# Kernel optimization log

Measured on AMD Instinct MI355X. Metric: run time of the kernel, lower is better.

## Reference

```python
import jax, jax.numpy as jnp
import numpy as np

B, S, P, D, H = 2, 1024, 1024, 2048, 16
DH = D // H
QMAX = 127.0


def quantize(x):
    # per-tensor abs-max int8 quantization, matching torch quantize(bits=8)
    scale = jnp.max(jnp.abs(x)) / QMAX
    x_q = jnp.clip(jnp.round(x / scale), -128.0, 127.0).astype(jnp.int8)
    return x_q, scale


def dequantize(x_q, scale):
    return x_q.astype(jnp.float32) * scale


def setup_inputs() -> dict:
    key = jax.random.key(0)
    ks = jax.random.split(key, 12)
    sd = 1.0 / np.sqrt(D)
    inp = {
        'hidden_states': jax.random.normal(ks[0], (B, S, D), jnp.float32),
        'Wq': jax.random.normal(ks[1], (D, D), jnp.float32) * sd,
        'bq': jnp.zeros((D,), jnp.float32),
        'Wk': jax.random.normal(ks[2], (D, D), jnp.float32) * sd,
        'bk': jnp.zeros((D,), jnp.float32),
        'Wv': jax.random.normal(ks[3], (D, D), jnp.float32) * sd,
        'bv': jnp.zeros((D,), jnp.float32),
        'Wo': jax.random.normal(ks[4], (D, D), jnp.float32) * sd,
        'bo': jnp.zeros((D,), jnp.float32),
        'past_k_q': jax.random.randint(ks[5], (B, P, D), -128, 128).astype(jnp.int8),
        'past_k_scale': jnp.float32(0.03),
        'past_v_q': jax.random.randint(ks[6], (B, P, D), -128, 128).astype(jnp.int8),
        'past_v_scale': jnp.float32(0.02),
    }
    return inp


def attention(h, k, v, Wq, bq, Wo, bo):
    # standard causal MHA; query positions are offset by the cache length P
    T = k.shape[1]  # P + S
    q = (h @ Wq + bq).reshape(B, S, H, DH)
    kh = k.reshape(B, T, H, DH)
    vh = v.reshape(B, T, H, DH)
    scores = jnp.einsum('bshd,bthd->bhst', q, kh) / np.sqrt(DH)  # [B,H,S,T]
    causal = jnp.arange(T)[None, :] <= (P + jnp.arange(S))[:, None]  # [S,T]
    scores = jnp.where(causal[None, None], scores, jnp.float32(-1e30))
    attn = jax.nn.softmax(scores, axis=-1)
    out = jnp.einsum('bhst,bthd->bshd', attn, vh).reshape(B, S, D)
    return out @ Wo + bo


def reference(hidden_states, Wq, bq, Wk, bk, Wv, bv, Wo, bo,
              past_k_q, past_k_scale, past_v_q, past_v_scale):
    k = hidden_states @ Wk + bk  # [B,S,D]
    v = hidden_states @ Wv + bv
    k_q, k_scale = quantize(k)
    v_q, v_scale = quantize(v)
    # dequantize cached KV and concat along the sequence dim (dim=1)
    k_prev = dequantize(past_k_q, past_k_scale)
    v_prev = dequantize(past_v_q, past_v_scale)
    k_full = jnp.concatenate([k_prev, k], axis=1)  # [B,P+S,D]
    v_full = jnp.concatenate([v_prev, v], axis=1)
    out = attention(hidden_states, k_full, v_full, Wq, bq, Wo, bo)
    return out, k_q, k_scale, v_q, v_scale
```

## Files before the change

kernel.cpp:

```cpp
#include <hip/hip_runtime.h>

#define SOFT_SCALE 0.08838834764831845f
#define BSD 4194304
#define NELEM 4194304

typedef __attribute__((ext_vector_type(4))) float    f32x4;
typedef __attribute__((ext_vector_type(8))) short    bf16x8;
typedef __attribute__((ext_vector_type(4))) short    bf16x4;
typedef __attribute__((ext_vector_type(4))) unsigned u32x4;

__device__ __forceinline__ float bs2f(short s) {
    unsigned u = ((unsigned)(unsigned short)s) << 16;
    return __builtin_bit_cast(float, u);
}
__device__ __forceinline__ short f2bs(float f) {
    unsigned u = __builtin_bit_cast(unsigned, f);
    unsigned r = (u + 0x7fffu + ((u >> 16) & 1u)) >> 16;
    return (short)r;
}

__device__ __forceinline__ void stage16(const short* g, short* l) {
#if __has_builtin(__builtin_amdgcn_global_load_lds)
    __builtin_amdgcn_global_load_lds(
        (const __attribute__((address_space(1))) void*)g,
        (__attribute__((address_space(3))) void*)l, 16, 0, 0);
#else
    *(bf16x8*)l = *(const bf16x8*)g;
#endif
}

__global__ void probe_init(const int* __restrict__ q, float* __restrict__ scal) {
    const int lane = threadIdx.x;
    int bad = 0;
#pragma unroll
    for (int i = 0; i < 4; ++i) {
        const int v = q[i * 64 + lane];
        bad |= (v < -128 || v > 127) ? 1 : 0;
    }
    const int anybad = __any(bad);
    if (lane == 0) ((int*)scal)[2] = anybad ? 0 : 1;
    if (lane == 1) scal[0] = 0.f;
    if (lane == 2) scal[1] = 0.f;
}

__global__ void prep_kernel(const float* __restrict__ X, short* __restrict__ Y,
                            const void* __restrict__ pk, const void* __restrict__ pv,
                            const float* __restrict__ psk, const float* __restrict__ psv,
                            short* __restrict__ Kf, short* __restrict__ Vf,
                            const int* __restrict__ wsflag) {
    const int z = blockIdx.z;
    const int stride = gridDim.x * blockDim.x;
    if (z == 0) {
        for (int i = blockIdx.x * blockDim.x + threadIdx.x; i < NELEM / 8; i += stride) {
            const int e = i * 8;
            f32x4 a = *(const f32x4*)&X[e];
            f32x4 b = *(const f32x4*)&X[e + 4];
            bf16x8 o;
            o[0] = f2bs(a[0]); o[1] = f2bs(a[1]); o[2] = f2bs(a[2]); o[3] = f2bs(a[3]);
            o[4] = f2bs(b[0]); o[5] = f2bs(b[1]); o[6] = f2bs(b[2]); o[7] = f2bs(b[3]);
            *(bf16x8*)&Y[e] = o;
        }
    } else {
        const void* src = (z == 2) ? pv : pk;
        const float sc = (z == 2) ? *psv : *psk;
        short* dst = (z == 2) ? Vf : Kf;
        const int flag = wsflag[2];
        for (int i = blockIdx.x * blockDim.x + threadIdx.x; i < NELEM / 8; i += stride) {
            const int e = i * 8;
            int vals[8];
            if (flag) {
                const int* s = (const int*)src + e;
                *(int4*)&vals[0] = *(const int4*)&s[0];
                *(int4*)&vals[4] = *(const int4*)&s[4];
            } else {
                const int2 wv = *(const int2*)((const char*)src + e);
#pragma unroll
                for (int j = 0; j < 4; ++j) vals[j] = (int)(signed char)(wv.x >> (8 * j));
#pragma unroll
                for (int j = 0; j < 4; ++j) vals[4 + j] = (int)(signed char)(wv.y >> (8 * j));
            }
            bf16x8 o;
#pragma unroll
            for (int j = 0; j < 8; ++j) o[j] = f2bs((float)vals[j] * sc);
            *(bf16x8*)&dst[e + ((e >> 21) << 21)] = o;
        }
    }
}

__global__ __launch_bounds__(256) void transpose_conv(const float* __restrict__ W0,
                                                      const float* __restrict__ W1,
                                                      const float* __restrict__ W2,
                                                      const float* __restrict__ W3,
                                                      short* __restrict__ WT) {
    __shared__ __align__(16) short Tl[64 * 68];
    const float* W = blockIdx.z == 0 ? W0 : (blockIdx.z == 1 ? W1 :
                     (blockIdx.z == 2 ? W2 : W3));
    short* out = WT + (long)blockIdx.z * 4194304;
    const int tid = threadIdx.x;
    const int n0 = blockIdx.x * 64, k0 = blockIdx.y * 64;
#pragma unroll
    for (int i = 0; i < 4; ++i) {
        const int e = i * 1024 + tid * 4;
        const int r = e >> 6, c = e & 63;
        f32x4 f = *(const f32x4*)&W[(long)(k0 + r) * 2048 + n0 + c];
        bf16x4 s4 = { f2bs(f[0]), f2bs(f[1]), f2bs(f[2]), f2bs(f[3]) };
        *(bf16x4*)&Tl[r * 68 + c] = s4;
    }
    __syncthreads();
#pragma unroll
    for (int i = 0; i < 4; ++i) {
        const int e = i * 1024 + tid * 4;
        const int nr = e >> 6, kk = e & 63;
        bf16x4 o = { Tl[(kk + 0) * 68 + nr], Tl[(kk + 1) * 68 + nr],
                     Tl[(kk + 2) * 68 + nr], Tl[(kk + 3) * 68 + nr] };
        *(bf16x4*)&out[(long)(n0 + nr) * 2048 + k0 + kk] = o;
    }
}

__global__ __launch_bounds__(512, 2) void gemm_qkv8(
    const short* __restrict__ A,
    const short* __restrict__ Bt0, const short* __restrict__ Bt1, const short* __restrict__ Bt2,
    const float* __restrict__ bi0, const float* __restrict__ bi1, const float* __restrict__ bi2,
    void* __restrict__ o0, void* __restrict__ o1, void* __restrict__ o2) {
    __shared__ __align__(16) short L[2][16384];

    const int orig = blockIdx.x + 8 * (blockIdx.y + 8 * blockIdx.z);
    int swz = (orig & 7) * 24 + (orig >> 3);
    const int bx = swz & 7; swz >>= 3;
    const int by = swz & 7;
    const int bz = swz >> 3;

    const short* Bt   = bz == 0 ? Bt0 : (bz == 1 ? Bt1 : Bt2);
    const float* bias = bz == 0 ? bi0 : (bz == 1 ? bi1 : bi2);
    void* outp        = bz == 0 ? o0  : (bz == 1 ? o1  : o2);
    const int mode    = (bz == 0) ? 1 : 2;
    const float scl   = (bz == 0) ? SOFT_SCALE : 1.f;

    const int tid = threadIdx.x, lane = tid & 63, w = tid >> 6;
    const int wm = w >> 2, wn = w & 3;
    const int l4 = lane >> 4, ln = lane & 15;
    const int m0 = by * 256, n0 = bx * 256;

    const int srow = tid >> 2;
    const int scol = (tid & 3) * 8;
    const short* gA0 = A  + (long)(m0 + srow) * 2048 + scol;
    const short* gA1 = A  + (long)(m0 + srow + 128) * 2048 + scol;
    const short* gB0 = Bt + (long)(n0 + srow) * 2048 + scol;
    const short* gB1 = Bt + (long)(n0 + srow + 128) * 2048 + scol;
    const int w0 = srow * 32 + (scol ^ ((srow & 3) << 3));

    const int aswz = (l4 * 8) ^ ((ln & 3) << 3);

    f32x4 acc[8][4];
#pragma unroll
    for (int mi = 0; mi < 8; ++mi)
#pragma unroll
        for (int ni = 0; ni < 4; ++ni) acc[mi][ni] = (f32x4){0, 0, 0, 0};

    bf16x8 g0, g1, g2, g3;
#define LOADG(t)                                   \
    do {                                           \
        const int ko = (t) * 32;                   \
        g0 = *(const bf16x8*)(gA0 + ko);           \
        g1 = *(const bf16x8*)(gA1 + ko);           \
        g2 = *(const bf16x8*)(gB0 + ko);           \
        g3 = *(const bf16x8*)(gB1 + ko);           \
    } while (0)
#define WRITEL(c)                                  \
    do {                                           \
        *(bf16x8*)&L[c][w0] = g0;                  \
        *(bf16x8*)&L[c][w0 + 4096] = g1;           \
        *(bf16x8*)&L[c][8192 + w0] = g2;           \
        *(bf16x8*)&L[c][8192 + w0 + 4096] = g3;    \
    } while (0)

    LOADG(0); WRITEL(0);
    LOADG(1); WRITEL(1);
    LOADG(2);
    __syncthreads();

    for (int s = 0; s < 64; ++s) {
        const int c = s & 1;
        bf16x8 af[8], bfq[4];
#pragma unroll
        for (int fm = 0; fm < 8; ++fm)
            af[fm] = *(const bf16x8*)&L[c][(wm * 128 + fm * 16 + ln) * 32 + aswz];
#pragma unroll
        for (int fn = 0; fn < 4; ++fn)
            bfq[fn] = *(const bf16x8*)&L[c][8192 + (wn * 64 + fn * 16 + ln) * 32 + aswz];
        __builtin_amdgcn_s_setprio(1);
#pragma unroll
        for (int fm = 0; fm < 8; ++fm)
#pragma unroll
            for (int fn = 0; fn < 4; ++fn)
                acc[fm][fn] = __builtin_amdgcn_mfma_f32_16x16x32_bf16(
                    af[fm], bfq[fn], acc[fm][fn], 0, 0, 0);
        __builtin_amdgcn_s_setprio(0);
        asm volatile("s_waitcnt lgkmcnt(0)" ::: "memory");
        __builtin_amdgcn_s_barrier();
        if (s < 62) WRITEL(c);
        if (s < 61) LOADG(s + 3);
        asm volatile("s_waitcnt lgkmcnt(0)" ::: "memory");
    }
#undef LOADG
#undef WRITEL

#pragma unroll
    for (int fn = 0; fn < 4; ++fn) {
        const int gn = n0 + wn * 64 + fn * 16 + ln;
        const float bv = bias[gn];
#pragma unroll
        for (int fm = 0; fm < 8; ++fm) {
#pragma unroll
            for (int r = 0; r < 4; ++r) {
                const int gm = m0 + wm * 128 + fm * 16 + l4 * 4 + r;
                const float v = (acc[fm][fn][r] + bv) * scl;
                if (mode == 1) {
                    ((short*)outp)[(long)gm * 2048 + gn] = f2bs(v);
                } else {
                    const int gr = gm + 1024 + ((gm >> 10) << 10);
                    ((short*)outp)[(long)gr * 2048 + gn] = f2bs(v);
                }
            }
        }
    }
}

__global__ __launch_bounds__(256, 2) void gemm_m97(
    const short* __restrict__ A, const short* __restrict__ Bt,
    const float* __restrict__ bias, void* __restrict__ outp,
    int mode, float scl) {
    __shared__ __align__(16) short Al[2][4096];
    __shared__ __align__(16) short Bl[2][4096];
    const int nbx = gridDim.x, nby = gridDim.y;
    const int nwg = nbx * nby;
    const int orig = blockIdx.x + nbx * blockIdx.y;
    const int cpx = nwg >> 3;
    int swz = (orig & 7) * cpx + (orig >> 3);
    const int bx = swz % nbx;
    const int by = swz / nbx;

    const int tid = threadIdx.x, lane = tid & 63, w = tid >> 6;
    const int wm = w >> 1, wn = w & 1, l4 = lane >> 4, ln = lane & 15;
    const int m0 = by * 128, n0 = bx * 128;

    const short* gA0 = A  + (long)(m0 + (tid >> 2)) * 2048 + (tid & 3) * 8;
    const short* gA1 = gA0 + 64 * 2048;
    const short* gB0 = Bt + (long)(n0 + (tid >> 2)) * 2048 + (tid & 3) * 8;
    const short* gB1 = gB0 + 64 * 2048;

    f32x4 acc[4][4];
#pragma unroll
    for (int mi = 0; mi < 4; ++mi)
#pragma unroll
        for (int ni = 0; ni < 4; ++ni) acc[mi][ni] = (f32x4){0, 0, 0, 0};

#define STAGE_G(buf, ko)                                   \
    do {                                                   \
        stage16(gA0 + (ko), &Al[buf][tid * 8]);            \
        stage16(gA1 + (ko), &Al[buf][2048 + tid * 8]);     \
        stage16(gB0 + (ko), &Bl[buf][tid * 8]);            \
        stage16(gB1 + (ko), &Bl[buf][2048 + tid * 8]);     \
    } while (0)

    STAGE_G(0, 0);
    asm volatile("s_waitcnt vmcnt(0)" ::: "memory");
    __syncthreads();
    int cur = 0;
    for (int kt = 0; kt < 64; ++kt) {
        if (kt < 63) STAGE_G(cur ^ 1, (kt + 1) * 32);
        bf16x8 af[4], bfr[4];
#pragma unroll
        for (int mi = 0; mi < 4; ++mi)
            af[mi] = *(const bf16x8*)&Al[cur][(wm * 64 + mi * 16 + ln) * 32 + l4 * 8];
#pragma unroll
        for (int ni = 0; ni < 4; ++ni)
            bfr[ni] = *(const bf16x8*)&Bl[cur][(wn * 64 + ni * 16 + ln) * 32 + l4 * 8];
#pragma unroll
        for (int mi = 0; mi < 4; ++mi)
#pragma unroll
            for (int ni = 0; ni < 4; ++ni)
                acc[mi][ni] = __builtin_amdgcn_mfma_f32_16x16x32_bf16(
                    af[mi], bfr[ni], acc[mi][ni], 0, 0, 0);
        asm volatile("s_waitcnt vmcnt(0)" ::: "memory");
        __syncthreads();
        cur ^= 1;
    }
#undef STAGE_G

#pragma unroll
    for (int ni = 0; ni < 4; ++ni) {
        const int gn = n0 + wn * 64 + ni * 16 + ln;
        const float bv = bias[gn];
#pragma unroll
        for (int mi = 0; mi < 4; ++mi) {
#pragma unroll
            for (int r = 0; r < 4; ++r) {
                const int gm = m0 + wm * 64 + mi * 16 + l4 * 4 + r;
                const float v = (acc[mi][ni][r] + bv) * scl;
                if (mode == 0) {
                    ((float*)outp)[(long)gm * 2048 + gn] = v;
                } else if (mode == 1) {
                    ((short*)outp)[(long)gm * 2048 + gn] = f2bs(v);
                } else {
                    const int gr = gm + 1024 + ((gm >> 10) << 10);
                    ((short*)outp)[(long)gr * 2048 + gn] = f2bs(v);
                }
            }
        }
    }
}

__global__ __launch_bounds__(256, 2) void gemm_wo(const short* __restrict__ A,
                                                  const short* __restrict__ Bt,
                                                  const float* __restrict__ bias,
                                                  float* __restrict__ outp) {
    __shared__ __align__(16) short Al[2][4096];
    __shared__ __align__(16) short Bl[2][2048];
    const int orig = blockIdx.x + 32 * blockIdx.y;
    const int swz = (orig & 7) * 64 + (orig >> 3);
    const int bx = swz & 31, by = swz >> 5;
    const int tid = threadIdx.x, lane = tid & 63, w = tid >> 6;
    const int wm = w >> 1, wn = w & 1, l4 = lane >> 4, ln = lane & 15;
    const int m0 = by * 128, n0 = bx * 64;

    const short* gA0 = A  + (long)(m0 + (tid >> 2)) * 2048 + (tid & 3) * 8;
    const short* gA1 = gA0 + 64 * 2048;
    const short* gB0 = Bt + (long)(n0 + (tid >> 2)) * 2048 + (tid & 3) * 8;

    f32x4 acc[4][2];
#pragma unroll
    for (int mi = 0; mi < 4; ++mi)
#pragma unroll
        for (int ni = 0; ni < 2; ++ni) acc[mi][ni] = (f32x4){0, 0, 0, 0};

#define STAGE_W(buf, ko)                                   \
    do {                                                   \
        stage16(gA0 + (ko), &Al[buf][tid * 8]);            \
        stage16(gA1 + (ko), &Al[buf][2048 + tid * 8]);     \
        stage16(gB0 + (ko), &Bl[buf][tid * 8]);            \
    } while (0)

    STAGE_W(0, 0);
    asm volatile("s_waitcnt vmcnt(0)" ::: "memory");
    __syncthreads();
    int cur = 0;
    for (int kt = 0; kt < 64; ++kt) {
        if (kt < 63) STAGE_W(cur ^ 1, (kt + 1) * 32);
        bf16x8 af[4], bfr[2];
#pragma unroll
        for (int mi = 0; mi < 4; ++mi)
            af[mi] = *(const bf16x8*)&Al[cur][(wm * 64 + mi * 16 + ln) * 32 + l4 * 8];
#pragma unroll
        for (int ni = 0; ni < 2; ++ni)
            bfr[ni] = *(const bf16x8*)&Bl[cur][(wn * 32 + ni * 16 + ln) * 32 + l4 * 8];
#pragma unroll
        for (int mi = 0; mi < 4; ++mi)
#pragma unroll
            for (int ni = 0; ni < 2; ++ni)
                acc[mi][ni] = __builtin_amdgcn_mfma_f32_16x16x32_bf16(
                    af[mi], bfr[ni], acc[mi][ni], 0, 0, 0);
        asm volatile("s_waitcnt vmcnt(0)" ::: "memory");
        __syncthreads();
        cur ^= 1;
    }
#undef STAGE_W

#pragma unroll
    for (int ni = 0; ni < 2; ++ni) {
        const int gn = n0 + wn * 32 + ni * 16 + ln;
        const float bv = bias[gn];
#pragma unroll
        for (int mi = 0; mi < 4; ++mi) {
#pragma unroll
            for (int r = 0; r < 4; ++r) {
                const int gm = m0 + wm * 64 + mi * 16 + l4 * 4 + r;
                outp[(long)gm * 2048 + gn] = acc[mi][ni][r] + bv;
            }
        }
    }
}

__global__ void absmax_kernel(const short* __restrict__ Kf, const short* __restrict__ Vf,
                              float* __restrict__ scal) {
    const int z = blockIdx.z;
    const short* src = z ? Vf : Kf;
    const int tid = threadIdx.x, lane = tid & 63, w = tid >> 6;
    float mx = 0.f;
    const int stride = gridDim.x * blockDim.x;
    for (int i = blockIdx.x * blockDim.x + tid; i < NELEM / 8; i += stride) {
        const int e = i * 8;
        const int flat = e + 2097152 + ((e >> 21) << 21);
        bf16x8 v = *(const bf16x8*)&src[flat];
#pragma unroll
        for (int j = 0; j < 8; ++j) mx = fmaxf(mx, fabsf(bs2f(v[j])));
    }
#pragma unroll
    for (int o = 32; o > 0; o >>= 1) mx = fmaxf(mx, __shfl_xor(mx, o));
    __shared__ float wred[4];
    if (lane == 0) wred[w] = mx;
    __syncthreads();
    if (tid == 0) {
        const float m2 = fmaxf(fmaxf(wred[0], wred[1]), fmaxf(wred[2], wred[3]));
        atomicMax((unsigned int*)&scal[z], __builtin_bit_cast(unsigned int, m2));
    }
}

__global__ void quantize_kernel(const short* __restrict__ Kf, const short* __restrict__ Vf,
                                const float* __restrict__ scal, float* __restrict__ out) {
    const int z = blockIdx.z;
    const short* src = z ? Vf : Kf;
    const float mx = scal[z];
    const float scale = mx * (1.f / 127.f);
    const float inv = (mx > 0.f) ? 127.f / mx : 0.f;
    const long ob = z ? (2L * BSD + 1) : (1L * BSD);
    if (blockIdx.x == 0 && threadIdx.x == 0)
        out[z ? (3L * BSD + 1) : (2L * BSD)] = scale;
    const int stride = gridDim.x * blockDim.x;
    for (int i = blockIdx.x * blockDim.x + threadIdx.x; i < NELEM / 4; i += stride) {
        const int e = i * 4;
        const int flat = e + 2097152 + ((e >> 21) << 21);
        bf16x4 x4 = *(const bf16x4*)&src[flat];
        float4 q;
        q.x = fminf(127.f, fmaxf(-128.f, rintf(bs2f(x4[0]) * inv)));
        q.y = fminf(127.f, fmaxf(-128.f, rintf(bs2f(x4[1]) * inv)));
        q.z = fminf(127.f, fmaxf(-128.f, rintf(bs2f(x4[2]) * inv)));
        q.w = fminf(127.f, fmaxf(-128.f, rintf(bs2f(x4[3]) * inv)));
        *(float4*)&out[ob + e] = q;
    }
}

__global__ __launch_bounds__(256, 2) void attn_kernel(const short* __restrict__ Q,
                                                      const short* __restrict__ Kf,
                                                      const short* __restrict__ Vf,
                                                      short* __restrict__ O) {
    __shared__ __align__(16) short Kl[2][64 * 136];
    __shared__ __align__(16) short Vt[2][128 * 72];
    const int L = blockIdx.x + 16 * (blockIdx.y + 16 * blockIdx.z);
    const int x = L & 7, rr = L >> 3;
    const int qt0 = rr & 15, pgrp = rr >> 4;
    const int p = x + 8 * pgrp;
    const int h = p >> 1, b = p & 1;
    const int qt = (pgrp >= 2) ? (15 - qt0) : qt0;

    const int tid = threadIdx.x, w = tid >> 6, lane = tid & 63;
    const int l4 = lane >> 4, n = lane & 15;
    const int rg = tid >> 4, cg = tid & 15, stc = cg * 8;
    const int sIdx = qt * 64 + w * 16 + n;
    const int qlim = 1024 + sIdx;

    bf16x8 qf[4];
#pragma unroll
    for (int c = 0; c < 4; ++c)
        qf[c] = *(const bf16x8*)&Q[(long)(b * 1024 + sIdx) * 2048 + h * 128 + c * 32 + l4 * 8];

    f32x4 acco[8];
#pragma unroll
    for (int i = 0; i < 8; ++i) acco[i] = (f32x4){0, 0, 0, 0};
    float m_run = 0.f, l_run = 0.f;

    const short* Kb = Kf + (long)(b * 2048) * 2048 + h * 128;
    const short* Vb = Vf + (long)(b * 2048) * 2048 + h * 128;
    const int nt = 17 + qt;

    bf16x8 kreg[4], vreg[4];
#define LOAD_KV(te)                                                                   \
    do {                                                                              \
        _Pragma("unroll")                                                             \
        for (int i = 0; i < 4; ++i)                                                   \
            kreg[i] = *(const bf16x8*)&Kb[(long)((te) + i * 16 + rg) * 2048 + stc];   \
        _Pragma("unroll")                                                             \
        for (int i = 0; i < 4; ++i)                                                   \
            vreg[i] = *(const bf16x8*)&Vb[(long)((te) + rg * 4 + i) * 2048 + stc];    \
    } while (0)
#define WRITE_BUF(bf)                                                                 \
    do {                                                                              \
        _Pragma("unroll")                                                             \
        for (int i = 0; i < 4; ++i)                                                   \
            *(bf16x8*)&Kl[bf][(i * 16 + rg) * 136 + stc] = kreg[i];                   \
        _Pragma("unroll")                                                             \
        for (int j = 0; j < 8; ++j) {                                                 \
            const int d = stc + j;                                                    \
            bf16x4 c4 = { vreg[0][j], vreg[1][j], vreg[2][j], vreg[3][j] };           \
            *(bf16x4*)&Vt[bf][d * 72 + ((rg ^ ((d >> 3) & 7)) << 2)] = c4;            \
        }                                                                             \
    } while (0)

    LOAD_KV(0);
    WRITE_BUF(0);
    __syncthreads();

    for (int t = 0; t < nt; ++t) {
        const int buf = t & 1;
        const int t0 = t * 64;
        if (t + 1 < nt) LOAD_KV((t + 1) * 64);

        float p16[16];
        __builtin_amdgcn_s_setprio(1);
#pragma unroll
        for (int kt = 0; kt < 4; ++kt) {
            f32x4 sc4 = (f32x4){0, 0, 0, 0};
#pragma unroll
            for (int c = 0; c < 4; ++c) {
                bf16x8 kfr = *(const bf16x8*)&Kl[buf][(kt * 16 + n) * 136 + c * 32 + l4 * 8];
                sc4 = __builtin_amdgcn_mfma_f32_16x16x32_bf16(kfr, qf[c], sc4, 0, 0, 0);
            }
#pragma unroll
            for (int r = 0; r < 4; ++r) p16[kt * 4 + r] = sc4[r];
        }
        __builtin_amdgcn_s_setprio(0);
        if (t >= 16) {
#pragma unroll
            for (int i = 0; i < 16; ++i) {
                const int kg = t0 + (i >> 2) * 16 + l4 * 4 + (i & 3);
                if (kg > qlim) p16[i] = -1e30f;
            }
        }

        float tmax = fmaxf(p16[0], p16[1]);
#pragma unroll
        for (int i = 2; i < 16; ++i) tmax = fmaxf(tmax, p16[i]);
        tmax = fmaxf(tmax, __shfl_xor(tmax, 16));
        tmax = fmaxf(tmax, __shfl_xor(tmax, 32));
        float e16[16], tsum = 0.f;
#pragma unroll
        for (int i = 0; i < 16; ++i) { e16[i] = __expf(p16[i] - m_run); tsum += e16[i]; }
        if (!__all(tmax <= m_run + 8.f)) {
            const float mnew = fmaxf(m_run, tmax);
            const float fac = __expf(m_run - mnew);
            tsum *= fac;
#pragma unroll
            for (int i = 0; i < 16; ++i) e16[i] *= fac;
            l_run *= fac;
#pragma unroll
            for (int i = 0; i < 8; ++i) acco[i] *= fac;
            m_run = mnew;
        }
        tsum += __shfl_xor(tsum, 16);
        tsum += __shfl_xor(tsum, 32);
        l_run += tsum;

        u32x4 pw0, pw1;
#pragma unroll
        for (int wd = 0; wd < 4; ++wd) {
            unsigned r0, r1;
            asm("v_cvt_pk_bf16_f32 %0, %1, %2" : "=v"(r0) : "v"(e16[2 * wd]), "v"(e16[2 * wd + 1]));
            asm("v_cvt_pk_bf16_f32 %0, %1, %2" : "=v"(r1) : "v"(e16[8 + 2 * wd]), "v"(e16[8 + 2 * wd + 1]));
            pw0[wd] = r0; pw1[wd] = r1;
        }
        bf16x8 pb[2] = { __builtin_bit_cast(bf16x8, pw0), __builtin_bit_cast(bf16x8, pw1) };

        __builtin_amdgcn_s_setprio(1);
#pragma unroll
        for (int dc = 0; dc < 8; ++dc) {
            const int d = dc * 16 + n;
            const int swd = ((d >> 3) & 7) << 2;
#pragma unroll
            for (int k32 = 0; k32 < 2; ++k32) {
                bf16x4 g0 = *(const bf16x4*)&Vt[buf][d * 72 + (k32 * 32 + ((4 * l4) ^ swd))];
                bf16x4 g1 = *(const bf16x4*)&Vt[buf][d * 72 + (k32 * 32 + ((16 + 4 * l4) ^ swd))];
                bf16x8 vf = { g0[0], g0[1], g0[2], g0[3], g1[0], g1[1], g1[2], g1[3] };
                acco[dc] = __builtin_amdgcn_mfma_f32_16x16x32_bf16(vf, pb[k32], acco[dc], 0, 0, 0);
            }
        }
        __builtin_amdgcn_s_setprio(0);

        if (t + 1 < nt) WRITE_BUF(buf ^ 1);
        __syncthreads();
    }
#undef LOAD_KV
#undef WRITE_BUF

    const float inv = 1.f / l_run;
#pragma unroll
    for (int dc = 0; dc < 8; ++dc)
#pragma unroll
        for (int r = 0; r < 4; ++r)
            Kl[0][(w * 16 + n) * 136 + dc * 16 + l4 * 4 + r] = f2bs(acco[dc][r] * inv);
    __syncthreads();
#pragma unroll
    for (int i = 0; i < 4; ++i) {
        const int row = i * 4 + (lane >> 4);
        const int col = (lane & 15) * 8;
        bf16x8 ov = *(const bf16x8*)&Kl[0][(w * 16 + row) * 136 + col];
        *(bf16x8*)&O[(long)(b * 1024 + qt * 64 + w * 16 + row) * 2048 + h * 128 + col] = ov;
    }
}

extern "C" void kernel_launch(void* const* d_in, const int* in_sizes, int n_in,
                              void* d_out, int out_size, void* d_ws, size_t ws_size,
                              hipStream_t stream) {
    const float* h   = (const float*)d_in[0];
    const float* Wq  = (const float*)d_in[1];
    const float* bq  = (const float*)d_in[2];
    const float* Wk  = (const float*)d_in[3];
    const float* bk  = (const float*)d_in[4];
    const float* Wv  = (const float*)d_in[5];
    const float* bv  = (const float*)d_in[6];
    const float* Wo  = (const float*)d_in[7];
    const float* bo  = (const float*)d_in[8];
    const void*  pkq = d_in[9];
    const float* pks = (const float*)d_in[10];
    const void*  pvq = d_in[11];
    const float* pvs = (const float*)d_in[12];
    float* out = (float*)d_out;

    char* ws = (char*)d_ws;
    dim3 blk(256);

    if (ws_size >= 83886336ull) {
        float* scal  = (float*)ws;
        short* hbf   = (short*)(ws + 256);
        short* WT4   = (short*)(ws + 256 + 1L * 8388608);
        short* Qbf   = (short*)(ws + 256 + 5L * 8388608);
        short* Kfull = (short*)(ws + 256 + 6L * 8388608);
        short* Vfull = (short*)(ws + 256 + 6L * 8388608 + 16777216);
        short* attnb = hbf;

        probe_init<<<1, 64, 0, stream>>>((const int*)pkq, scal);
        prep_kernel<<<dim3(256, 1, 3), blk, 0, stream>>>(h, hbf, pkq, pvq, pks, pvs,
                                                         Kfull, Vfull, (const int*)d_ws);
        transpose_conv<<<dim3(32, 32, 4), blk, 0, stream>>>(Wq, Wk, Wv, Wo, WT4);
        gemm_qkv8<<<dim3(8, 8, 3), dim3(512), 0, stream>>>(hbf, WT4, WT4 + 4194304,
                                                           WT4 + 8388608, bq, bk, bv,
                                                           Qbf, Kfull, Vfull);
        absmax_kernel<<<dim3(512, 1, 2), blk, 0, stream>>>(Kfull, Vfull, scal);
        quantize_kernel<<<dim3(256, 1, 2), blk, 0, stream>>>(Kfull, Vfull, scal, out);
        attn_kernel<<<dim3(16, 16, 2), blk, 0, stream>>>(Qbf, Kfull, Vfull, attnb);
        gemm_wo<<<dim3(32, 16), blk, 0, stream>>>(attnb, WT4 + 12582912, bo, out);
    } else {
        float* scal  = (float*)ws;
        short* hbf   = (short*)(ws + 256);
        short* WT    = (short*)(ws + 256 + 1L * 8388608);
        short* Qbf   = (short*)(ws + 256 + 2L * 8388608);
        short* Kfull = (short*)(ws + 256 + 3L * 8388608);
        short* Vfull = (short*)(ws + 256 + 3L * 8388608 + 16777216);
        short* attnb = hbf;

        probe_init<<<1, 64, 0, stream>>>((const int*)pkq, scal);
        prep_kernel<<<dim3(256, 1, 3), blk, 0, stream>>>(h, hbf, pkq, pvq, pks, pvs,
                                                         Kfull, Vfull, (const int*)d_ws);
        transpose_conv<<<dim3(32, 32, 1), blk, 0, stream>>>(Wk, Wk, Wk, Wk, WT);
        gemm_m97<<<dim3(16, 16), blk, 0, stream>>>(hbf, WT, bk, Kfull, 2, 1.f);
        transpose_conv<<<dim3(32, 32, 1), blk, 0, stream>>>(Wv, Wv, Wv, Wv, WT);
        gemm_m97<<<dim3(16, 16), blk, 0, stream>>>(hbf, WT, bv, Vfull, 2, 1.f);
        absmax_kernel<<<dim3(512, 1, 2), blk, 0, stream>>>(Kfull, Vfull, scal);
        quantize_kernel<<<dim3(256, 1, 2), blk, 0, stream>>>(Kfull, Vfull, scal, out);
        transpose_conv<<<dim3(32, 32, 1), blk, 0, stream>>>(Wq, Wq, Wq, Wq, WT);
        gemm_m97<<<dim3(16, 16), blk, 0, stream>>>(hbf, WT, bq, Qbf, 1, SOFT_SCALE);
        attn_kernel<<<dim3(16, 16, 2), blk, 0, stream>>>(Qbf, Kfull, Vfull, attnb);
        transpose_conv<<<dim3(32, 32, 1), blk, 0, stream>>>(Wo, Wo, Wo, Wo, WT);
        gemm_wo<<<dim3(32, 16), blk, 0, stream>>>(attnb, WT, bo, out);
    }
}
```

Baseline: 219.0 us.

## Switch QKV GEMM to direct global-to-LDS loads with 4-stage pipeline

```diff
diff --git a/kernel.cpp b/kernel.cpp
--- a/kernel.cpp
+++ b/kernel.cpp
@@ -122,7 +122,7 @@
     const short* __restrict__ Bt0, const short* __restrict__ Bt1, const short* __restrict__ Bt2,
     const float* __restrict__ bi0, const float* __restrict__ bi1, const float* __restrict__ bi2,
     void* __restrict__ o0, void* __restrict__ o1, void* __restrict__ o2) {
-    __shared__ __align__(16) short L[2][16384];
+    __shared__ __align__(16) short L[4][16384];
 
     const int orig = blockIdx.x + 8 * (blockIdx.y + 8 * blockIdx.z);
     int swz = (orig & 7) * 24 + (orig >> 3);
@@ -141,15 +141,22 @@
     const int l4 = lane >> 4, ln = lane & 15;
     const int m0 = by * 256, n0 = bx * 256;
 
-    const int srow = tid >> 2;
     const int scol = (tid & 3) * 8;
-    const short* gA0 = A  + (long)(m0 + srow) * 2048 + scol;
-    const short* gA1 = A  + (long)(m0 + srow + 128) * 2048 + scol;
-    const short* gB0 = Bt + (long)(n0 + srow) * 2048 + scol;
-    const short* gB1 = Bt + (long)(n0 + srow + 128) * 2048 + scol;
-    const int w0 = srow * 32 + (scol ^ ((srow & 3) << 3));
-
-    const int aswz = (l4 * 8) ^ ((ln & 3) << 3);
+    const short* gA = A  + (long)(m0 + (tid >> 2)) * 2048 + scol;
+    const short* gB = Bt + (long)(n0 + (tid >> 2)) * 2048 + scol;
+
+#define ISSUE_A(t)                                                        \
+    do {                                                                  \
+        const long ko = (long)(t) * 32;                                   \
+        stage16(gA + ko,              &L[(t) & 3][tid * 8]);              \
+        stage16(gA + ko + 128 * 2048, &L[(t) & 3][4096 + tid * 8]);       \
+    } while (0)
+#define ISSUE_B(t)                                                        \
+    do {                                                                  \
+        const long ko = (long)(t) * 32;                                   \
+        stage16(gB + ko,              &L[(t) & 3][8192 + tid * 8]);       \
+        stage16(gB + ko + 128 * 2048, &L[(t) & 3][12288 + tid * 8]);      \
+    } while (0)
 
     f32x4 acc[8][4];
 #pragma unroll
@@ -157,53 +164,53 @@
 #pragma unroll
         for (int ni = 0; ni < 4; ++ni) acc[mi][ni] = (f32x4){0, 0, 0, 0};
 
-    bf16x8 g0, g1, g2, g3;
-#define LOADG(t)                                   \
-    do {                                           \
-        const int ko = (t) * 32;                   \
-        g0 = *(const bf16x8*)(gA0 + ko);           \
-        g1 = *(const bf16x8*)(gA1 + ko);           \
-        g2 = *(const bf16x8*)(gB0 + ko);           \
-        g3 = *(const bf16x8*)(gB1 + ko);           \
-    } while (0)
-#define WRITEL(c)                                  \
-    do {                                           \
-        *(bf16x8*)&L[c][w0] = g0;                  \
-        *(bf16x8*)&L[c][w0 + 4096] = g1;           \
-        *(bf16x8*)&L[c][8192 + w0] = g2;           \
-        *(bf16x8*)&L[c][8192 + w0 + 4096] = g3;    \
-    } while (0)
-
-    LOADG(0); WRITEL(0);
-    LOADG(1); WRITEL(1);
-    LOADG(2);
-    __syncthreads();
-
-    for (int s = 0; s < 64; ++s) {
-        const int c = s & 1;
-        bf16x8 af[8], bfq[4];
-#pragma unroll
-        for (int fm = 0; fm < 8; ++fm)
-            af[fm] = *(const bf16x8*)&L[c][(wm * 128 + fm * 16 + ln) * 32 + aswz];
+    ISSUE_A(0); ISSUE_B(0);
+    ISSUE_A(1); ISSUE_B(1);
+    ISSUE_A(2); ISSUE_B(2);
+
+    for (int t = 0; t < 64; ++t) {
+        if (t < 62)       asm volatile("s_waitcnt vmcnt(8)" ::: "memory");
+        else if (t == 62) asm volatile("s_waitcnt vmcnt(4)" ::: "memory");
+        else              asm volatile("s_waitcnt vmcnt(0)" ::: "memory");
+        __builtin_amdgcn_s_barrier();
+        const int c = t & 3;
+        const short* Ab = &L[c][0];
+        const short* Bb = &L[c][8192];
+
+        bf16x8 bf[4], af[4];
 #pragma unroll
         for (int fn = 0; fn < 4; ++fn)
-            bfq[fn] = *(const bf16x8*)&L[c][8192 + (wn * 64 + fn * 16 + ln) * 32 + aswz];
+            bf[fn] = *(const bf16x8*)&Bb[(wn * 64 + fn * 16 + ln) * 32 + l4 * 8];
+#pragma unroll
+        for (int fm = 0; fm < 4; ++fm)
+            af[fm] = *(const bf16x8*)&Ab[(wm * 128 + fm * 16 + ln) * 32 + l4 * 8];
+        if (t + 3 < 64) ISSUE_A(t + 3);
         __builtin_amdgcn_s_setprio(1);
 #pragma unroll
-        for (int fm = 0; fm < 8; ++fm)
+        for (int fm = 0; fm < 4; ++fm)
 #pragma unroll
             for (int fn = 0; fn < 4; ++fn)
                 acc[fm][fn] = __builtin_amdgcn_mfma_f32_16x16x32_bf16(
-                    af[fm], bfq[fn], acc[fm][fn], 0, 0, 0);
+                    af[fm], bf[fn], acc[fm][fn], 0, 0, 0);
         __builtin_amdgcn_s_setprio(0);
-        asm volatile("s_waitcnt lgkmcnt(0)" ::: "memory");
         __builtin_amdgcn_s_barrier();
-        if (s < 62) WRITEL(c);
-        if (s < 61) LOADG(s + 3);
-        asm volatile("s_waitcnt lgkmcnt(0)" ::: "memory");
-    }
-#undef LOADG
-#undef WRITEL
+
+        bf16x8 af2[4];
+#pragma unroll
+        for (int fm = 0; fm < 4; ++fm)
+            af2[fm] = *(const bf16x8*)&Ab[(wm * 128 + 64 + fm * 16 + ln) * 32 + l4 * 8];
+        if (t + 3 < 64) ISSUE_B(t + 3);
+        __builtin_amdgcn_s_setprio(1);
+#pragma unroll
+        for (int fm = 0; fm < 4; ++fm)
+#pragma unroll
+            for (int fn = 0; fn < 4; ++fn)
+                acc[4 + fm][fn] = __builtin_amdgcn_mfma_f32_16x16x32_bf16(
+                    af2[fm], bf[fn], acc[4 + fm][fn], 0, 0, 0);
+        __builtin_amdgcn_s_setprio(0);
+    }
+#undef ISSUE_A
+#undef ISSUE_B
 
 #pragma unroll
     for (int fn = 0; fn < 4; ++fn) {
```

Result: no change. 215.8 us (-1.5%).
